# Optimization experiments

Hardware: AMD Instinct MI355X
Metric: run time of the kernel (lower is better)

Reference implementation:

```python
import jax, jax.numpy as jnp
import numpy as np

N_CLASSES = 40
EMBED_DIM = 128
MOMENTUM = 0.1
LAMBDA_R, LAMBDA_C, LAMBDA_M = 1.0, 0.5, 1.0
BATCH = 262144


def setup_inputs() -> dict:
    key = jax.random.key(0)
    k1, k2, k3 = jax.random.split(key, 3)
    z = jax.random.normal(k1, (BATCH, EMBED_DIM), dtype=jnp.float32)
    y = jax.random.randint(k2, (BATCH,), 0, N_CLASSES)
    centers = jax.random.normal(k3, (N_CLASSES, EMBED_DIM), dtype=jnp.float32)
    initialized = jnp.ones((N_CLASSES,), dtype=bool)
    # buffers derived from class_counts (imbalanced ramp), r0=gamma=m0=1, alpha=0.25
    counts = jnp.asarray([1000.0 * (i + 1) for i in range(N_CLASSES)], jnp.float32)
    n_max = jnp.max(counts)
    target_radii = 1.0 + 1.0 * jnp.log(n_max / (counts + 1.0))
    margins = 1.0 * jnp.power(n_max / (counts + 1.0), 0.25)
    return {"z": z, "y": y, "centers": centers, "initialized": initialized,
            "target_radii": target_radii, "margins": margins}


def _update_centers(z, y, centers, initialized):
    # EMA centroid update on detached embeddings (torch.no_grad equivalent).
    zs = jax.lax.stop_gradient(z)
    sums = jax.ops.segment_sum(zs, y, num_segments=N_CLASSES)            # [C, D]
    cnt = jax.ops.segment_sum(jnp.ones((zs.shape[0],), zs.dtype), y,
                              num_segments=N_CLASSES)                    # [C]
    mean = sums / jnp.maximum(cnt, 1.0)[:, None]
    ema = (1.0 - MOMENTUM) * centers + MOMENTUM * mean
    new = jnp.where(initialized[:, None], ema, mean)                     # first-touch init
    return jnp.where((cnt > 0)[:, None], new, centers)                   # skip empty classes


def reference(z, y, centers, initialized, target_radii, margins):
    c = _update_centers(z, y, centers, initialized)                      # [C, D]

    # radial loss: smooth L1 (beta=1) between ||z|| and per-class target radius
    r = jnp.linalg.norm(z, axis=-1)                                      # [B]
    d = r - target_radii[y]
    ad = jnp.abs(d)
    loss_radial = jnp.mean(jnp.where(ad < 1.0, 0.5 * d * d, ad - 0.5))

    # compact loss: mean squared distance to own centroid
    diff = z - c[y]                                                      # [B, D]
    loss_compact = jnp.mean(jnp.sum(diff * diff, axis=-1))

    # margin loss: min distance to any other class centroid via Gram trick
    z2 = jnp.sum(z * z, axis=-1)                                         # [B]
    c2 = jnp.sum(c * c, axis=-1)                                         # [C]
    d2 = z2[:, None] + c2[None, :] - 2.0 * (z @ c.T)                     # [B, C]
    dist = jnp.sqrt(jnp.maximum(d2, 0.0))
    own = y[:, None] == jnp.arange(N_CLASSES)[None, :]                   # [B, C] bool
    dist_opp = jnp.min(jnp.where(own, jnp.inf, dist), axis=1)            # [B]
    loss_margin = jnp.mean(jax.nn.relu(margins[y] - dist_opp))

    return LAMBDA_R * loss_radial + LAMBDA_C * loss_compact + LAMBDA_M * loss_margin
```

## Files before the change

kernel.cpp:

```cpp
#include <hip/hip_runtime.h>
#include <math.h>

#define BATCH 262144
#define DIM   128
#define NCLS  40
#define NCP   48
#define CD    (NCLS * DIM)

#define TB1 256
#define NB1 256
#define TB3 256
#define NB3 (BATCH / 256)

typedef __attribute__((ext_vector_type(8))) short short8;
typedef __attribute__((ext_vector_type(4))) float f32x4;

__device__ __forceinline__ short f2bf(float f) {
    unsigned u = __float_as_uint(f);
    u += 0x7fffu + ((u >> 16) & 1u);
    return (short)(u >> 16);
}

#define K1_ALL(M) M(0) M(1) M(2) M(3) M(4) M(5) M(6) M(7) M(8) M(9) \
                  M(10) M(11) M(12) M(13) M(14) M(15) M(16) M(17) M(18) M(19) \
                  M(20) M(21) M(22) M(23) M(24) M(25) M(26) M(27) M(28) M(29) \
                  M(30) M(31) M(32) M(33) M(34) M(35) M(36) M(37) M(38) M(39)
#define K1_DECL(c) float2 a##c = {0.0f, 0.0f};
#define K1_CASE(c) case c: a##c.x += v.x; a##c.y += v.y; break;
#define K1_ST0(c)  s_buf[(c) * 64 + lane] = a##c;
#define K1_RMW(c)  { float2 t_ = s_buf[(c) * 64 + lane];                     \
                     t_.x += a##c.x; t_.y += a##c.y;                         \
                     s_buf[(c) * 64 + lane] = t_; }

__global__ __launch_bounds__(TB1) void k1_segsum(const float* __restrict__ z,
                                                 const int* __restrict__ y,
                                                 float* __restrict__ ps,
                                                 float* __restrict__ gcnt) {
    __shared__ float2 s_buf[NCLS * 64];
    __shared__ float  s_cnt[NCLS];
    const int t = threadIdx.x;
    if (t < NCLS) s_cnt[t] = 0.0f;
    __syncthreads();

    const int w     = t >> 6;
    const int lane  = t & 63;
    const int rbase = blockIdx.x * 1024 + w * 256;

    const int yA = y[rbase + lane];
    const int yB = y[rbase + 64 + lane];
    const int yC = y[rbase + 128 + lane];
    const int yD = y[rbase + 192 + lane];
    atomicAdd(&s_cnt[yA], 1.0f);
    atomicAdd(&s_cnt[yB], 1.0f);
    atomicAdd(&s_cnt[yC], 1.0f);
    atomicAdd(&s_cnt[yD], 1.0f);

    const float* __restrict__ zp = z + (size_t)rbase * DIM + lane * 2;

    float2 vb[16];
#pragma unroll
    for (int q = 0; q < 16; ++q) vb[q] = *(const float2*)(zp + (size_t)q * DIM);

    K1_ALL(K1_DECL)

#pragma unroll 1
    for (int jj = 0; jj < 4; ++jj) {
        int yj = yA;
        if (jj == 1) yj = yB;
        if (jj == 2) yj = yC;
        if (jj == 3) yj = yD;
#pragma unroll 1
        for (int i0 = 0; i0 < 64; i0 += 16) {
#pragma unroll
            for (int q = 0; q < 16; ++q) {
                const int i = jj * 64 + i0 + q;
                const float2 v = vb[q];
                int sn = i + 16;
                if (sn > 255) sn = i;
                vb[q] = *(const float2*)(zp + (size_t)sn * DIM);
                const int cls = __builtin_amdgcn_readlane(yj, i0 + q);
                switch (cls) { K1_ALL(K1_CASE) default: break; }
            }
        }
    }

    if (w == 0) { K1_ALL(K1_ST0) }
    __syncthreads();
    if (w == 1) { K1_ALL(K1_RMW) }
    __syncthreads();
    if (w == 2) { K1_ALL(K1_RMW) }
    __syncthreads();
    if (w == 3) { K1_ALL(K1_RMW) }
    __syncthreads();

    float2* __restrict__ psb = (float2*)(ps + (size_t)blockIdx.x * CD);
    for (int i = t; i < NCLS * 64; i += TB1) psb[i] = s_buf[i];
    if (t < NCLS) atomicAdd(&gcnt[t], s_cnt[t]);
}

__global__ __launch_bounds__(512) void k2_centers(const float* __restrict__ part_sums,
                                                  const float* __restrict__ gcnt,
                                                  const float* __restrict__ centers,
                                                  short* __restrict__ cbf,
                                                  float* __restrict__ c2_out) {
    const int j  = blockIdx.x;
    const int t  = threadIdx.x;
    const int d  = t & 127;
    const int qr = t >> 7;

    if (j >= NCLS) {
        if (qr == 0) cbf[j * DIM + d] = 0;
        if (t == 0) c2_out[j] = 1e30f;
        return;
    }

    const float* __restrict__ p = part_sums + j * DIM + d + (size_t)(qr * 64) * CD;
    float s = 0.0f;
#pragma unroll 8
    for (int b = 0; b < 64; ++b) s += p[(size_t)b * CD];

    __shared__ float red[512];
    red[t] = s;
    __syncthreads();

    float cv = 0.0f;
    if (qr == 0) {
        const float ssum = red[d] + red[d + 128] + red[d + 256] + red[d + 384];
        const float cnt  = gcnt[j];
        const float mean = ssum / fmaxf(cnt, 1.0f);
        const float ctr  = centers[j * DIM + d];
        const float ema  = 0.9f * ctr + 0.1f * mean;
        cv = (cnt > 0.0f) ? ema : ctr;
        cbf[j * DIM + d] = f2bf(cv);
    }
    __syncthreads();
    red[t] = cv * cv;
    __syncthreads();
    for (int off = 256; off > 0; off >>= 1) {
        if (t < off) red[t] += red[t + off];
        __syncthreads();
    }
    if (t == 0) c2_out[j] = red[0];
}

__global__ __launch_bounds__(TB3) void k3_loss(const float* __restrict__ z,
                                               const int* __restrict__ y,
                                               const short* __restrict__ cbf,
                                               const float* __restrict__ c2,
                                               const float* __restrict__ tr,
                                               const float* __restrict__ mg,
                                               float* __restrict__ out) {
    __shared__ float s_S[4][64 * 52];
    __shared__ float s_c2[NCP];

    const int t = threadIdx.x;
    if (t < NCP) s_c2[t] = c2[t];

    const int w    = t >> 6;
    const int lane = t & 63;
    const int q    = lane >> 4;
    const int col  = lane & 15;
    const int wavebase = blockIdx.x * 256 + w * 64;

    short8 bfrag[3][4];
#pragma unroll
    for (int ct = 0; ct < 3; ++ct)
#pragma unroll
        for (int s = 0; s < 4; ++s)
            bfrag[ct][s] = *(const short8*)(cbf + (ct * 16 + col) * DIM + s * 32 + q * 8);

    __syncthreads();

#pragma unroll 1
    for (int rt = 0; rt < 4; ++rt) {
        const float* __restrict__ zrow =
            z + (size_t)(wavebase + rt * 16 + col) * DIM + q * 8;

        float4 f[8];
#pragma unroll
        for (int s = 0; s < 4; ++s) {
            f[2 * s]     = *(const float4*)(zrow + s * 32);
            f[2 * s + 1] = *(const float4*)(zrow + s * 32 + 4);
        }

        float zp = 0.0f;
#pragma unroll
        for (int i = 0; i < 8; ++i) {
            zp = fmaf(f[i].x, f[i].x, zp);
            zp = fmaf(f[i].y, f[i].y, zp);
            zp = fmaf(f[i].z, f[i].z, zp);
            zp = fmaf(f[i].w, f[i].w, zp);
        }

        short8 afr[4];
#pragma unroll
        for (int s = 0; s < 4; ++s) {
            const float4 f0 = f[2 * s], f1 = f[2 * s + 1];
            afr[s][0] = f2bf(f0.x); afr[s][1] = f2bf(f0.y);
            afr[s][2] = f2bf(f0.z); afr[s][3] = f2bf(f0.w);
            afr[s][4] = f2bf(f1.x); afr[s][5] = f2bf(f1.y);
            afr[s][6] = f2bf(f1.z); afr[s][7] = f2bf(f1.w);
        }

        f32x4 acc0 = {0.f, 0.f, 0.f, 0.f};
        f32x4 acc1 = {0.f, 0.f, 0.f, 0.f};
        f32x4 acc2 = {0.f, 0.f, 0.f, 0.f};
#pragma unroll
        for (int s = 0; s < 4; ++s) {
            acc0 = __builtin_amdgcn_mfma_f32_16x16x32_bf16(afr[s], bfrag[0][s], acc0, 0, 0, 0);
            acc1 = __builtin_amdgcn_mfma_f32_16x16x32_bf16(afr[s], bfrag[1][s], acc1, 0, 0, 0);
            acc2 = __builtin_amdgcn_mfma_f32_16x16x32_bf16(afr[s], bfrag[2][s], acc2, 0, 0, 0);
        }

        zp += __shfl_xor(zp, 16);
        zp += __shfl_xor(zp, 32);
        if (q == 0) s_S[w][(rt * 16 + col) * 52 + 48] = zp;

#pragma unroll
        for (int reg = 0; reg < 4; ++reg) {
            const int rr = rt * 16 + q * 4 + reg;
            s_S[w][rr * 52 + col]      = acc0[reg];
            s_S[w][rr * 52 + 16 + col] = acc1[reg];
            s_S[w][rr * 52 + 32 + col] = acc2[reg];
        }
    }

    const int row = blockIdx.x * 256 + t;
    const int cls = y[row];
    const float z2v = s_S[w][lane * 52 + 48];

    float own_d2 = 0.0f;
    float mind2  = 3.4e38f;
#pragma unroll
    for (int k = 0; k < 12; ++k) {
        const float4 Sv = *(const float4*)&s_S[w][lane * 52 + 4 * k];
        const float Se[4] = {Sv.x, Sv.y, Sv.z, Sv.w};
#pragma unroll
        for (int e = 0; e < 4; ++e) {
            const int j = 4 * k + e;
            float d2 = fmaxf(z2v + s_c2[j] - 2.0f * Se[e], 0.0f);
            const bool isown = (j == cls);
            own_d2 = isown ? d2 : own_d2;
            mind2  = isown ? mind2 : fminf(mind2, d2);
        }
    }

    const float r  = sqrtf(z2v);
    const float dd = r - tr[cls];
    const float ad = fabsf(dd);
    const float rad = (ad < 1.0f) ? 0.5f * dd * dd : ad - 0.5f;

    const float dist = sqrtf(mind2);
    const float marg = fmaxf(mg[cls] - dist, 0.0f);

    const float tot = rad + 0.5f * own_d2 + marg;

    __syncthreads();
    float* s_red = &s_S[0][0];
    s_red[t] = tot;
    __syncthreads();
    for (int off = TB3 / 2; off > 0; off >>= 1) {
        if (t < off) s_red[t] += s_red[t + off];
        __syncthreads();
    }
    if (t == 0) atomicAdd(out, s_red[0] * (1.0f / (float)BATCH));
}

extern "C" void kernel_launch(void* const* d_in, const int* in_sizes, int n_in,
                              void* d_out, int out_size, void* d_ws, size_t ws_size,
                              hipStream_t stream) {
    const float* z       = (const float*)d_in[0];
    const int*   y       = (const int*)d_in[1];
    const float* centers = (const float*)d_in[2];
    const float* tr      = (const float*)d_in[4];
    const float* mg      = (const float*)d_in[5];
    float* out = (float*)d_out;

    float* ws        = (float*)d_ws;
    float* part_sums = ws;
    float* c2buf     = part_sums + (size_t)NB1 * CD;
    float* gcnt      = c2buf + NCP;
    short* cbf       = (short*)(gcnt + NCLS);

    hipMemsetAsync(gcnt, 0, NCLS * sizeof(float), stream);
    hipMemsetAsync(out, 0, sizeof(float), stream);

    k1_segsum<<<NB1, TB1, 0, stream>>>(z, y, part_sums, gcnt);
    k2_centers<<<NCP, 512, 0, stream>>>(part_sums, gcnt, centers, cbf, c2buf);
    k3_loss<<<NB3, TB3, 0, stream>>>(z, y, cbf, c2buf, tr, mg, out);
}
```

Measured before the change: 261.1 us.

## Stream segment-sum rows via async global-to-LDS ring and split center reduction

The segment-sum kernel now runs 512 threads per block, each wave owning 128 rows. Rows are staged into an 8-deep LDS ring with global_load_lds and explicit vmcnt waits, replacing the per-lane register prefetch, so memory latency overlaps with the class-switch accumulation. The cross-wave reduction uses two LDS buffers, halving the serialized read-modify-write steps. The centers kernel splits each class over two blocks, writing partial c2 values that the loss kernel sums. This adds LDS pressure and depends on correct asm waitcnt ordering.

Measured after the change: 274.7 us. +5.2%, slower.

```diff
diff --git a/kernel.cpp b/kernel.cpp
--- a/kernel.cpp
+++ b/kernel.cpp
@@ -7,7 +7,7 @@
 #define NCP   48
 #define CD    (NCLS * DIM)
 
-#define TB1 256
+#define TB1 512
 #define NB1 256
 #define TB3 256
 #define NB3 (BATCH / 256)
@@ -26,127 +26,157 @@
                   M(20) M(21) M(22) M(23) M(24) M(25) M(26) M(27) M(28) M(29) \
                   M(30) M(31) M(32) M(33) M(34) M(35) M(36) M(37) M(38) M(39)
 #define K1_DECL(c) float2 a##c = {0.0f, 0.0f};
-#define K1_CASE(c) case c: a##c.x += v.x; a##c.y += v.y; break;
-#define K1_ST0(c)  s_buf[(c) * 64 + lane] = a##c;
-#define K1_RMW(c)  { float2 t_ = s_buf[(c) * 64 + lane];                     \
-                     t_.x += a##c.x; t_.y += a##c.y;                         \
-                     s_buf[(c) * 64 + lane] = t_; }
+#define K1_CASE(c) case c: a##c.x += vv.x; a##c.y += vv.y; \
+    asm volatile("" : "+v"(a##c.x), "+v"(a##c.y)); break;
+#define K1_ACCUM(CLS, V) { const float2 vv = (V); \
+    switch (CLS) { K1_ALL(K1_CASE) default: break; } }
+#define K1_STA(c)  s_bufA[(c) * 64 + lane] = a##c;
+#define K1_STB(c)  s_bufB[(c) * 64 + lane] = a##c;
+#define K1_RMWA(c) { float2 t_ = s_bufA[(c) * 64 + lane]; \
+                     t_.x += a##c.x; t_.y += a##c.y; \
+                     s_bufA[(c) * 64 + lane] = t_; }
+#define K1_RMWB(c) { float2 t_ = s_bufB[(c) * 64 + lane]; \
+                     t_.x += a##c.x; t_.y += a##c.y; \
+                     s_bufB[(c) * 64 + lane] = t_; }
+
+__device__ __forceinline__ void k1_stage(const float* src, float* dst) {
+    __builtin_amdgcn_global_load_lds(
+        (const __attribute__((address_space(1))) void*)src,
+        (__attribute__((address_space(3))) void*)dst, 16, 0, 0);
+}
 
 __global__ __launch_bounds__(TB1) void k1_segsum(const float* __restrict__ z,
                                                  const int* __restrict__ y,
                                                  float* __restrict__ ps,
                                                  float* __restrict__ gcnt) {
-    __shared__ float2 s_buf[NCLS * 64];
+    __shared__ float  s_ring[8][8 * 256];
+    __shared__ float2 s_bufA[NCLS * 64];
+    __shared__ float2 s_bufB[NCLS * 64];
     __shared__ float  s_cnt[NCLS];
-    const int t = threadIdx.x;
+
+    const int t    = threadIdx.x;
+    const int w    = t >> 6;
+    const int lane = t & 63;
     if (t < NCLS) s_cnt[t] = 0.0f;
     __syncthreads();
 
-    const int w     = t >> 6;
-    const int lane  = t & 63;
-    const int rbase = blockIdx.x * 1024 + w * 256;
-
-    const int yA = y[rbase + lane];
-    const int yB = y[rbase + 64 + lane];
-    const int yC = y[rbase + 128 + lane];
-    const int yD = y[rbase + 192 + lane];
-    atomicAdd(&s_cnt[yA], 1.0f);
-    atomicAdd(&s_cnt[yB], 1.0f);
-    atomicAdd(&s_cnt[yC], 1.0f);
-    atomicAdd(&s_cnt[yD], 1.0f);
-
-    const float* __restrict__ zp = z + (size_t)rbase * DIM + lane * 2;
-
-    float2 vb[16];
-#pragma unroll
-    for (int q = 0; q < 16; ++q) vb[q] = *(const float2*)(zp + (size_t)q * DIM);
+    const int rbase = blockIdx.x * 1024 + w * 128;
+
+    const int2 y2 = *(const int2*)(y + rbase + lane * 2);
+    atomicAdd(&s_cnt[y2.x], 1.0f);
+    atomicAdd(&s_cnt[y2.y], 1.0f);
+
+    const float* __restrict__ zw = z + (size_t)rbase * DIM;
+    float* __restrict__ ringw = s_ring[w];
+
+#pragma unroll
+    for (int p = 0; p < 8; ++p)
+        k1_stage(zw + (size_t)p * 256 + lane * 4, ringw + p * 256);
 
     K1_ALL(K1_DECL)
 
 #pragma unroll 1
-    for (int jj = 0; jj < 4; ++jj) {
-        int yj = yA;
-        if (jj == 1) yj = yB;
-        if (jj == 2) yj = yC;
-        if (jj == 3) yj = yD;
-#pragma unroll 1
-        for (int i0 = 0; i0 < 64; i0 += 16) {
-#pragma unroll
-            for (int q = 0; q < 16; ++q) {
-                const int i = jj * 64 + i0 + q;
-                const float2 v = vb[q];
-                int sn = i + 16;
-                if (sn > 255) sn = i;
-                vb[q] = *(const float2*)(zp + (size_t)sn * DIM);
-                const int cls = __builtin_amdgcn_readlane(yj, i0 + q);
-                switch (cls) { K1_ALL(K1_CASE) default: break; }
-            }
-        }
-    }
-
-    if (w == 0) { K1_ALL(K1_ST0) }
-    __syncthreads();
-    if (w == 1) { K1_ALL(K1_RMW) }
-    __syncthreads();
-    if (w == 2) { K1_ALL(K1_RMW) }
-    __syncthreads();
-    if (w == 3) { K1_ALL(K1_RMW) }
+    for (int p = 0; p < 56; ++p) {
+        asm volatile("s_waitcnt vmcnt(7)" ::: "memory");
+        __builtin_amdgcn_sched_barrier(0);
+        const int slot = p & 7;
+        const float2 v0 = *(const float2*)(ringw + slot * 256 + lane * 2);
+        const float2 v1 = *(const float2*)(ringw + slot * 256 + 128 + lane * 2);
+        const int c0 = __builtin_amdgcn_readlane(y2.x, p);
+        const int c1 = __builtin_amdgcn_readlane(y2.y, p);
+        K1_ACCUM(c0, v0)
+        K1_ACCUM(c1, v1)
+        k1_stage(zw + (size_t)(p + 8) * 256 + lane * 4, ringw + slot * 256);
+    }
+
+#define K1_TAIL(P, W) { \
+        asm volatile("s_waitcnt vmcnt(" #W ")" ::: "memory"); \
+        __builtin_amdgcn_sched_barrier(0); \
+        const int slot = (P) & 7; \
+        const float2 v0 = *(const float2*)(ringw + slot * 256 + lane * 2); \
+        const float2 v1 = *(const float2*)(ringw + slot * 256 + 128 + lane * 2); \
+        const int c0 = __builtin_amdgcn_readlane(y2.x, (P)); \
+        const int c1 = __builtin_amdgcn_readlane(y2.y, (P)); \
+        K1_ACCUM(c0, v0) \
+        K1_ACCUM(c1, v1) }
+    K1_TAIL(56, 7) K1_TAIL(57, 6) K1_TAIL(58, 5) K1_TAIL(59, 4)
+    K1_TAIL(60, 3) K1_TAIL(61, 2) K1_TAIL(62, 1) K1_TAIL(63, 0)
+#undef K1_TAIL
+
+    __syncthreads();
+    if (w == 0) { K1_ALL(K1_STA) }
+    if (w == 1) { K1_ALL(K1_STB) }
+    __syncthreads();
+    if (w == 2) { K1_ALL(K1_RMWA) }
+    if (w == 3) { K1_ALL(K1_RMWB) }
+    __syncthreads();
+    if (w == 4) { K1_ALL(K1_RMWA) }
+    if (w == 5) { K1_ALL(K1_RMWB) }
+    __syncthreads();
+    if (w == 6) { K1_ALL(K1_RMWA) }
+    if (w == 7) { K1_ALL(K1_RMWB) }
     __syncthreads();
 
     float2* __restrict__ psb = (float2*)(ps + (size_t)blockIdx.x * CD);
-    for (int i = t; i < NCLS * 64; i += TB1) psb[i] = s_buf[i];
+    for (int i = t; i < NCLS * 64; i += TB1) {
+        const float2 A = s_bufA[i], B = s_bufB[i];
+        psb[i] = make_float2(A.x + B.x, A.y + B.y);
+    }
     if (t < NCLS) atomicAdd(&gcnt[t], s_cnt[t]);
 }
 
-__global__ __launch_bounds__(512) void k2_centers(const float* __restrict__ part_sums,
+__global__ __launch_bounds__(512) void k2_centers(const float* __restrict__ ps,
                                                   const float* __restrict__ gcnt,
                                                   const float* __restrict__ centers,
                                                   short* __restrict__ cbf,
-                                                  float* __restrict__ c2_out) {
-    const int j  = blockIdx.x;
-    const int t  = threadIdx.x;
-    const int d  = t & 127;
-    const int qr = t >> 7;
+                                                  float* __restrict__ c2p) {
+    const int j    = blockIdx.x >> 1;
+    const int half = blockIdx.x & 1;
+    const int t    = threadIdx.x;
+    const int dl   = t & 63;
+    const int d    = half * 64 + dl;
+    const int s    = t >> 6;
 
     if (j >= NCLS) {
-        if (qr == 0) cbf[j * DIM + d] = 0;
-        if (t == 0) c2_out[j] = 1e30f;
+        if (s == 0) cbf[j * DIM + d] = 0;
+        if (t == 0) c2p[blockIdx.x] = 5e29f;
         return;
     }
 
-    const float* __restrict__ p = part_sums + j * DIM + d + (size_t)(qr * 64) * CD;
-    float s = 0.0f;
+    const float* __restrict__ p = ps + j * DIM + d + (size_t)(s * 32) * CD;
+    float sum = 0.0f;
 #pragma unroll 8
-    for (int b = 0; b < 64; ++b) s += p[(size_t)b * CD];
+    for (int b = 0; b < 32; ++b) sum += p[(size_t)b * CD];
 
     __shared__ float red[512];
-    red[t] = s;
-    __syncthreads();
-
-    float cv = 0.0f;
-    if (qr == 0) {
-        const float ssum = red[d] + red[d + 128] + red[d + 256] + red[d + 384];
+    red[t] = sum;
+    __syncthreads();
+
+    if (s == 0) {
+        float tot = 0.0f;
+#pragma unroll
+        for (int k = 0; k < 8; ++k) tot += red[(k << 6) | dl];
         const float cnt  = gcnt[j];
-        const float mean = ssum / fmaxf(cnt, 1.0f);
+        const float mean = tot / fmaxf(cnt, 1.0f);
         const float ctr  = centers[j * DIM + d];
         const float ema  = 0.9f * ctr + 0.1f * mean;
-        cv = (cnt > 0.0f) ? ema : ctr;
+        const float cv   = (cnt > 0.0f) ? ema : ctr;
         cbf[j * DIM + d] = f2bf(cv);
-    }
-    __syncthreads();
-    red[t] = cv * cv;
-    __syncthreads();
-    for (int off = 256; off > 0; off >>= 1) {
-        if (t < off) red[t] += red[t + off];
-        __syncthreads();
-    }
-    if (t == 0) c2_out[j] = red[0];
+        red[t] = cv * cv;
+    }
+    __syncthreads();
+    if (t == 0) {
+        float sc = 0.0f;
+#pragma unroll 8
+        for (int i = 0; i < 64; ++i) sc += red[i];
+        c2p[blockIdx.x] = sc;
+    }
 }
 
 __global__ __launch_bounds__(TB3) void k3_loss(const float* __restrict__ z,
                                                const int* __restrict__ y,
                                                const short* __restrict__ cbf,
-                                               const float* __restrict__ c2,
+                                               const float* __restrict__ c2p,
                                                const float* __restrict__ tr,
                                                const float* __restrict__ mg,
                                                float* __restrict__ out) {
@@ -154,7 +184,7 @@
     __shared__ float s_c2[NCP];
 
     const int t = threadIdx.x;
-    if (t < NCP) s_c2[t] = c2[t];
+    if (t < NCP) s_c2[t] = c2p[2 * t] + c2p[2 * t + 1];
 
     const int w    = t >> 6;
     const int lane = t & 63;
@@ -278,14 +308,14 @@
 
     float* ws        = (float*)d_ws;
     float* part_sums = ws;
-    float* c2buf     = part_sums + (size_t)NB1 * CD;
-    float* gcnt      = c2buf + NCP;
+    float* c2p       = part_sums + (size_t)NB1 * CD;
+    float* gcnt      = c2p + 2 * NCP;
     short* cbf       = (short*)(gcnt + NCLS);
 
     hipMemsetAsync(gcnt, 0, NCLS * sizeof(float), stream);
     hipMemsetAsync(out, 0, sizeof(float), stream);
 
     k1_segsum<<<NB1, TB1, 0, stream>>>(z, y, part_sums, gcnt);
-    k2_centers<<<NCP, 512, 0, stream>>>(part_sums, gcnt, centers, cbf, c2buf);
-    k3_loss<<<NB3, TB3, 0, stream>>>(z, y, cbf, c2buf, tr, mg, out);
-}
+    k2_centers<<<2 * NCP, 512, 0, stream>>>(part_sums, gcnt, centers, cbf, c2p);
+    k3_loss<<<NB3, TB3, 0, stream>>>(z, y, cbf, c2p, tr, mg, out);
+}
```
